# Optimization experiments

Hardware: AMD Instinct MI355X
Metric: run time of the kernel (lower is better)

The kernel has to match this reference:

```python
import jax, jax.numpy as jnp
import numpy as np

N_NODES = 100000

def _graph_conv(x, src, dst, W, b, num_nodes):
    # DGL GraphConv, norm='both', edge_weight=None:
    # h = D_in^{-1/2} * A * (D_out^{-1/2} * x @ W) + b
    ones = jnp.ones(src.shape[0], dtype=x.dtype)
    out_deg = jax.ops.segment_sum(ones, src, num_segments=num_nodes)
    in_deg = jax.ops.segment_sum(ones, dst, num_segments=num_nodes)
    norm_src = jax.lax.rsqrt(jnp.clip(out_deg, 1.0))  # [N]
    norm_dst = jax.lax.rsqrt(jnp.clip(in_deg, 1.0))   # [N]
    h = (x * norm_src[:, None]) @ W                    # [N, out] (weight first: in>=out)
    msg = h[src]                                       # gather over edges [E, out]
    agg = jax.ops.segment_sum(msg, dst, num_segments=num_nodes)  # scatter-add [N, out]
    return agg * norm_dst[:, None] + b


def setup_inputs() -> dict:
    key = jax.random.key(0)
    k = jax.random.split(key, 8)
    N, F, H, C, E = N_NODES, 512, 16, 40, 3200000
    x = jax.random.normal(k[0], (N, F), dtype=jnp.float32)
    edge_src = jax.random.randint(k[1], (E,), 0, N, dtype=jnp.int32)
    edge_dst = jax.random.randint(k[2], (E,), 0, N, dtype=jnp.int32)
    # Glorot-style init for GraphConv weights, zero bias (DGL defaults)
    W1 = jax.random.normal(k[3], (F, H), dtype=jnp.float32) * (1.0 / np.sqrt(F))
    b1 = jnp.zeros((H,), dtype=jnp.float32)
    W2 = jax.random.normal(k[4], (H, C), dtype=jnp.float32) * (1.0 / np.sqrt(H))
    b2 = jnp.zeros((C,), dtype=jnp.float32)
    return {"x": x, "edge_src": edge_src, "edge_dst": edge_dst,
            "W1": W1, "b1": b1, "W2": W2, "b2": b2}


def reference(x, edge_src, edge_dst, W1, b1, W2, b2):
    h = _graph_conv(x, edge_src, edge_dst, W1, b1, N_NODES)
    h = jax.nn.relu(h)
    # dropout p=0.5 is identity in eval mode
    out = _graph_conv(h, edge_src, edge_dst, W2, b2, N_NODES)
    return out
```

## Files before the change

kernel.cpp:

```cpp
#include <hip/hip_runtime.h>

#define F_IN  512
#define H_DIM 16
#define C_OUT 40
#define NBLK_P 256

static inline size_t align_up(size_t x, size_t a) { return (x + a - 1) / a * a; }

__global__ __launch_bounds__(256) void k_pcount(const int* __restrict__ src,
        const int* __restrict__ dst, int E, int chunk, int nbk,
        int* __restrict__ histS, int* __restrict__ histT) {
    __shared__ int hs[512], hd[512];
    for (int i = threadIdx.x; i < 512; i += 256) { hs[i] = 0; hd[i] = 0; }
    __syncthreads();
    int b = blockIdx.x;
    int s = b * chunk, e = min(s + chunk, E);
    for (int i = s + threadIdx.x; i < e; i += 256) {
        atomicAdd(&hs[src[i] >> 8], 1);
        atomicAdd(&hd[dst[i] >> 8], 1);
    }
    __syncthreads();
    for (int i = threadIdx.x; i < nbk; i += 256) {
        histS[i * NBLK_P + b] = hs[i];
        histT[i * NBLK_P + b] = hd[i];
    }
}

__global__ void k_scan1(int* __restrict__ histS, int* __restrict__ histT,
                        int* __restrict__ bsums) {
    __shared__ int tmp[256];
    int* h = blockIdx.y ? histT : histS;
    int* bs = bsums + blockIdx.y * 512;
    int t = threadIdx.x;
    int gid = blockIdx.x * 256 + t;
    int v = h[gid];
    tmp[t] = v;
    __syncthreads();
    for (int off = 1; off < 256; off <<= 1) {
        int add = (t >= off) ? tmp[t - off] : 0;
        __syncthreads();
        tmp[t] += add;
        __syncthreads();
    }
    h[gid] = tmp[t] - v;
    if (t == 255) bs[blockIdx.x] = tmp[255];
}

__global__ void k_scan2(int* __restrict__ bsums, int nb) {
    __shared__ int tmp[512];
    int* bs = bsums + blockIdx.x * 512;
    int t = threadIdx.x;
    int v = (t < nb) ? bs[t] : 0;
    tmp[t] = v;
    __syncthreads();
    for (int off = 1; off < 512; off <<= 1) {
        int add = (t >= off) ? tmp[t - off] : 0;
        __syncthreads();
        tmp[t] += add;
        __syncthreads();
    }
    if (t < nb) bs[t] = tmp[t] - v;
}

__global__ void k_scan3(int* __restrict__ histS, int* __restrict__ histT,
                        const int* __restrict__ bsums) {
    int* h = blockIdx.y ? histT : histS;
    const int* bs = bsums + blockIdx.y * 512;
    h[blockIdx.x * 256 + threadIdx.x] += bs[blockIdx.x];
}

__global__ __launch_bounds__(256) void k_pscat(const int* __restrict__ src,
        const int* __restrict__ dst, int E, int chunk,
        const int* __restrict__ histS, const int* __restrict__ histT,
        unsigned char* __restrict__ srcb, unsigned int* __restrict__ pairsb) {
    __shared__ int cs[512], cd[512];
    for (int i = threadIdx.x; i < 512; i += 256) { cs[i] = 0; cd[i] = 0; }
    __syncthreads();
    int b = blockIdx.x;
    int s = b * chunk, e = min(s + chunk, E);
    for (int i = s + threadIdx.x; i < e; i += 256) {
        int k = src[i];
        int d = dst[i];
        int bks = k >> 8;
        int bkd = d >> 8;
        int rs = atomicAdd(&cs[bks], 1);
        int rd = atomicAdd(&cd[bkd], 1);
        srcb[histS[bks * NBLK_P + b] + rs] = (unsigned char)(k & 255);
        pairsb[histT[bkd * NBLK_P + b] + rd] =
            (unsigned int)k | ((unsigned int)(d & 255) << 24);
    }
}

__global__ __launch_bounds__(256) void k_bbuild(const unsigned char* __restrict__ srcb,
        const unsigned int* __restrict__ pairsb,
        const int* __restrict__ histS, const int* __restrict__ histT,
        int nbk, int E, int N, int* __restrict__ outdeg,
        int* __restrict__ indeg, int* __restrict__ csroff, int* __restrict__ csrsrc) {
    __shared__ int h[256], offs[256], cnt[256], tmp[256];
    int t = threadIdx.x, b = blockIdx.x;
    int node = (b << 8) + t;

    int sstart = histS[b * NBLK_P];
    int send = (b + 1 < nbk) ? histS[(b + 1) * NBLK_P] : E;
    h[t] = 0;
    __syncthreads();
    for (int i = sstart + t; i < send; i += 256)
        atomicAdd(&h[srcb[i]], 1);
    __syncthreads();
    if (node < N) outdeg[node] = h[t];
    __syncthreads();

    int bstart = histT[b * NBLK_P];
    int bend = (b + 1 < nbk) ? histT[(b + 1) * NBLK_P] : E;
    h[t] = 0; cnt[t] = 0;
    __syncthreads();
    for (int i = bstart + t; i < bend; i += 256)
        atomicAdd(&h[pairsb[i] >> 24], 1);
    __syncthreads();
    int v = h[t];
    tmp[t] = v;
    __syncthreads();
    for (int off = 1; off < 256; off <<= 1) {
        int add = (t >= off) ? tmp[t - off] : 0;
        __syncthreads();
        tmp[t] += add;
        __syncthreads();
    }
    offs[t] = tmp[t] - v;
    __syncthreads();
    if (node < N) {
        indeg[node] = v;
        csroff[node] = bstart + offs[t];
    }
    for (int i = bstart + t; i < bend; i += 256) {
        unsigned int p = pairsb[i];
        int l = p >> 24;
        int r = atomicAdd(&cnt[l], 1);
        csrsrc[bstart + offs[l] + r] = (int)(p & 0xFFFFFF);
    }
}

__global__ __launch_bounds__(256) void k_gemm1(const float* __restrict__ x,
        const float* __restrict__ W1, const int* __restrict__ outdeg,
        float* __restrict__ h1, int n) {
    __shared__ float Ws[F_IN * H_DIM];
    for (int i = threadIdx.x; i < F_IN * H_DIM / 4; i += 256)
        ((float4*)Ws)[i] = ((const float4*)W1)[i];
    __syncthreads();

    int row = blockIdx.x * 256 + threadIdx.x;
    if (row >= n) return;
    const float4* xr = (const float4*)(x + (size_t)row * F_IN);
    float ns = rsqrtf(fmaxf((float)outdeg[row], 1.f));

    float acc[H_DIM];
#pragma unroll
    for (int j = 0; j < H_DIM; ++j) acc[j] = 0.f;

    for (int c = 0; c < F_IN / 16; ++c) {
        float4 xv0 = xr[c * 4 + 0];
        float4 xv1 = xr[c * 4 + 1];
        float4 xv2 = xr[c * 4 + 2];
        float4 xv3 = xr[c * 4 + 3];
        float xs[16] = {xv0.x, xv0.y, xv0.z, xv0.w,
                        xv1.x, xv1.y, xv1.z, xv1.w,
                        xv2.x, xv2.y, xv2.z, xv2.w,
                        xv3.x, xv3.y, xv3.z, xv3.w};
#pragma unroll
        for (int kk = 0; kk < 16; ++kk) {
            const float* wr = &Ws[(c * 16 + kk) * H_DIM];
#pragma unroll
            for (int j = 0; j < H_DIM; ++j) acc[j] += xs[kk] * wr[j];
        }
    }

    float4* o = (float4*)(h1 + (size_t)row * H_DIM);
#pragma unroll
    for (int qq = 0; qq < 4; ++qq)
        o[qq] = make_float4(acc[qq * 4 + 0] * ns, acc[qq * 4 + 1] * ns,
                            acc[qq * 4 + 2] * ns, acc[qq * 4 + 3] * ns);
}

__global__ __launch_bounds__(256) void k_agg1(const int* __restrict__ csroff,
        const int* __restrict__ indeg, const int* __restrict__ outdeg,
        const int* __restrict__ csrsrc, const float* __restrict__ h1,
        const float* __restrict__ b1, float* __restrict__ g, int n) {
    int t = threadIdx.x;
    int q = t & 3;
    int lv = t >> 2;
    int v = blockIdx.x * 64 + lv;
    if (v >= n) return;
    int start = csroff[v];
    int len = indeg[v];
    const float4* h4 = (const float4*)h1;
    float4 acc = make_float4(0.f, 0.f, 0.f, 0.f);
    int i = 0;
    for (; i + 4 <= len; i += 4) {
        int s0 = csrsrc[start + i + 0];
        int s1 = csrsrc[start + i + 1];
        int s2 = csrsrc[start + i + 2];
        int s3 = csrsrc[start + i + 3];
        float4 m0 = h4[(size_t)s0 * 4 + q];
        float4 m1 = h4[(size_t)s1 * 4 + q];
        float4 m2 = h4[(size_t)s2 * 4 + q];
        float4 m3 = h4[(size_t)s3 * 4 + q];
        acc.x += m0.x + m1.x + m2.x + m3.x;
        acc.y += m0.y + m1.y + m2.y + m3.y;
        acc.z += m0.z + m1.z + m2.z + m3.z;
        acc.w += m0.w + m1.w + m2.w + m3.w;
    }
    for (; i < len; ++i) {
        int s = csrsrc[start + i];
        float4 m = h4[(size_t)s * 4 + q];
        acc.x += m.x; acc.y += m.y; acc.z += m.z; acc.w += m.w;
    }
    float nd = rsqrtf(fmaxf((float)len, 1.f));
    float ns = rsqrtf(fmaxf((float)outdeg[v], 1.f));
    float4 bb = ((const float4*)b1)[q];
    float4 r;
    r.x = fmaxf(acc.x * nd + bb.x, 0.f) * ns;
    r.y = fmaxf(acc.y * nd + bb.y, 0.f) * ns;
    r.z = fmaxf(acc.z * nd + bb.z, 0.f) * ns;
    r.w = fmaxf(acc.w * nd + bb.w, 0.f) * ns;
    ((float4*)g)[(size_t)v * 4 + q] = r;
}

__global__ __launch_bounds__(256) void k_agg2(const int* __restrict__ csroff,
        const int* __restrict__ indeg, const int* __restrict__ csrsrc,
        const float* __restrict__ gbuf, const float* __restrict__ W2,
        const float* __restrict__ b2, float* __restrict__ out, int n) {
    __shared__ float Ws[H_DIM * C_OUT];
    __shared__ float agg[64][17];
    int t = threadIdx.x;
    for (int i = t; i < H_DIM * C_OUT; i += 256) Ws[i] = W2[i];

    int q = t & 3;
    int lv = t >> 2;
    int v = blockIdx.x * 64 + lv;
    float4 acc = make_float4(0.f, 0.f, 0.f, 0.f);
    if (v < n) {
        int start = csroff[v];
        int len = indeg[v];
        const float4* g4 = (const float4*)gbuf;
        int i = 0;
        for (; i + 4 <= len; i += 4) {
            int s0 = csrsrc[start + i + 0];
            int s1 = csrsrc[start + i + 1];
            int s2 = csrsrc[start + i + 2];
            int s3 = csrsrc[start + i + 3];
            float4 m0 = g4[(size_t)s0 * 4 + q];
            float4 m1 = g4[(size_t)s1 * 4 + q];
            float4 m2 = g4[(size_t)s2 * 4 + q];
            float4 m3 = g4[(size_t)s3 * 4 + q];
            acc.x += m0.x + m1.x + m2.x + m3.x;
            acc.y += m0.y + m1.y + m2.y + m3.y;
            acc.z += m0.z + m1.z + m2.z + m3.z;
            acc.w += m0.w + m1.w + m2.w + m3.w;
        }
        for (; i < len; ++i) {
            int s = csrsrc[start + i];
            float4 m = g4[(size_t)s * 4 + q];
            acc.x += m.x; acc.y += m.y; acc.z += m.z; acc.w += m.w;
        }
    }
    agg[lv][q * 4 + 0] = acc.x;
    agg[lv][q * 4 + 1] = acc.y;
    agg[lv][q * 4 + 2] = acc.z;
    agg[lv][q * 4 + 3] = acc.w;
    __syncthreads();

    for (int idx = t; idx < 64 * C_OUT; idx += 256) {
        int dlv = idx / C_OUT;
        int c = idx % C_OUT;
        int dv = blockIdx.x * 64 + dlv;
        if (dv < n) {
            float s = 0.f;
#pragma unroll
            for (int k = 0; k < H_DIM; ++k) s += agg[dlv][k] * Ws[k * C_OUT + c];
            float nd = rsqrtf(fmaxf((float)indeg[dv], 1.f));
            out[(size_t)dv * C_OUT + c] = s * nd + b2[c];
        }
    }
}

extern "C" void kernel_launch(void* const* d_in, const int* in_sizes, int n_in,
                              void* d_out, int out_size, void* d_ws, size_t ws_size,
                              hipStream_t stream) {
    const float* x  = (const float*)d_in[0];
    const int* esrc = (const int*)d_in[1];
    const int* edst = (const int*)d_in[2];
    const float* W1 = (const float*)d_in[3];
    const float* b1 = (const float*)d_in[4];
    const float* W2 = (const float*)d_in[5];
    const float* b2 = (const float*)d_in[6];
    float* out = (float*)d_out;

    const int N = in_sizes[0] / F_IN;
    const int E = in_sizes[1];
    const int nbk = (N + 255) >> 8;
    const int chunk = (E + NBLK_P - 1) / NBLK_P;

    char* p = (char*)d_ws;
    auto alloc = [&](size_t bytes) -> char* {
        char* r = p; p += align_up(bytes, 256); return r;
    };
    int*  histS  = (int*)alloc((size_t)nbk * NBLK_P * 4);
    int*  histT  = (int*)alloc((size_t)nbk * NBLK_P * 4);
    int*  bsums  = (int*)alloc(1024 * 4);
    unsigned int*  pairsb = (unsigned int*)alloc((size_t)E * 4);
    unsigned char* srcb   = (unsigned char*)alloc((size_t)E);
    int*  csrsrc = (int*)alloc((size_t)E * 4);
    int*  indeg  = (int*)alloc((size_t)N * 4);
    int*  outdeg = (int*)alloc((size_t)N * 4);
    int*  csroff = (int*)alloc((size_t)N * 4);

    float* h1 = (float*)pairsb;
    float* g  = h1 + (size_t)N * H_DIM;

    k_pcount<<<NBLK_P, 256, 0, stream>>>(esrc, edst, E, chunk, nbk, histS, histT);
    k_scan1<<<dim3(nbk, 2), 256, 0, stream>>>(histS, histT, bsums);
    k_scan2<<<2, 512, 0, stream>>>(bsums, nbk);
    k_scan3<<<dim3(nbk, 2), 256, 0, stream>>>(histS, histT, bsums);
    k_pscat<<<NBLK_P, 256, 0, stream>>>(esrc, edst, E, chunk, histS, histT,
                                        srcb, pairsb);
    k_bbuild<<<nbk, 256, 0, stream>>>(srcb, pairsb, histS, histT, nbk, E, N,
                                      outdeg, indeg, csroff, csrsrc);

    k_gemm1<<<(N + 255) / 256, 256, 0, stream>>>(x, W1, outdeg, h1, N);
    int nb64 = (N + 63) / 64;
    k_agg1<<<nb64, 256, 0, stream>>>(csroff, indeg, outdeg, csrsrc, h1, b1, g, N);
    k_agg2<<<nb64, 256, 0, stream>>>(csroff, indeg, csrsrc, g, W2, b2, out, N);
}
```

Measured before the change: 279.6 us.

## Fuse edge histogram with first GEMM and fold scan3 into consumers

The dense x@W1 GEMM now runs as extra blocks inside the edge histogram kernel, so the compute-heavy GEMM overlaps with the atomic-bound counting pass and no longer waits for degrees. The out-degree normalisation moves into k_bbuild, which rescales h1 in place. The scan3 pass is removed: consumers add the block sums on the fly. The partition count doubles to 512, and h1 gets its own buffer instead of aliasing pairsb. The cost is an extra read-modify-write of h1 and extra index arithmetic in the scatter.

```diff
diff --git a/kernel.cpp b/kernel.cpp
--- a/kernel.cpp
+++ b/kernel.cpp
@@ -3,34 +3,78 @@
 #define F_IN  512
 #define H_DIM 16
 #define C_OUT 40
-#define NBLK_P 256
+#define NBLK_P 512
 
 static inline size_t align_up(size_t x, size_t a) { return (x + a - 1) / a * a; }
 
-__global__ __launch_bounds__(256) void k_pcount(const int* __restrict__ src,
+__global__ __launch_bounds__(256) void k_fused1(const int* __restrict__ src,
         const int* __restrict__ dst, int E, int chunk, int nbk,
-        int* __restrict__ histS, int* __restrict__ histT) {
-    __shared__ int hs[512], hd[512];
-    for (int i = threadIdx.x; i < 512; i += 256) { hs[i] = 0; hd[i] = 0; }
-    __syncthreads();
-    int b = blockIdx.x;
-    int s = b * chunk, e = min(s + chunk, E);
-    for (int i = s + threadIdx.x; i < e; i += 256) {
-        atomicAdd(&hs[src[i] >> 8], 1);
-        atomicAdd(&hd[dst[i] >> 8], 1);
-    }
-    __syncthreads();
-    for (int i = threadIdx.x; i < nbk; i += 256) {
-        histS[i * NBLK_P + b] = hs[i];
-        histT[i * NBLK_P + b] = hd[i];
-    }
+        int* __restrict__ histS, int* __restrict__ histT,
+        const float* __restrict__ x, const float* __restrict__ W1,
+        float* __restrict__ h1, int n) {
+    __shared__ float smem[F_IN * H_DIM];
+    int t = threadIdx.x;
+
+    if (blockIdx.x < NBLK_P) {
+        int* hs = (int*)smem;
+        int* hd = hs + 512;
+        for (int i = t; i < 1024; i += 256) hs[i] = 0;
+        __syncthreads();
+        int b = blockIdx.x;
+        int s = b * chunk, e = min(s + chunk, E);
+        for (int i = s + t; i < e; i += 256) {
+            atomicAdd(&hs[src[i] >> 8], 1);
+            atomicAdd(&hd[dst[i] >> 8], 1);
+        }
+        __syncthreads();
+        for (int i = t; i < nbk; i += 256) {
+            histS[i * NBLK_P + b] = hs[i];
+            histT[i * NBLK_P + b] = hd[i];
+        }
+        return;
+    }
+
+    for (int i = t; i < F_IN * H_DIM / 4; i += 256)
+        ((float4*)smem)[i] = ((const float4*)W1)[i];
+    __syncthreads();
+
+    int row = (blockIdx.x - NBLK_P) * 256 + t;
+    if (row >= n) return;
+    const float4* xr = (const float4*)(x + (size_t)row * F_IN);
+
+    float acc[H_DIM];
+#pragma unroll
+    for (int j = 0; j < H_DIM; ++j) acc[j] = 0.f;
+
+    for (int c = 0; c < F_IN / 16; ++c) {
+        float4 xv0 = xr[c * 4 + 0];
+        float4 xv1 = xr[c * 4 + 1];
+        float4 xv2 = xr[c * 4 + 2];
+        float4 xv3 = xr[c * 4 + 3];
+        float xs[16] = {xv0.x, xv0.y, xv0.z, xv0.w,
+                        xv1.x, xv1.y, xv1.z, xv1.w,
+                        xv2.x, xv2.y, xv2.z, xv2.w,
+                        xv3.x, xv3.y, xv3.z, xv3.w};
+#pragma unroll
+        for (int kk = 0; kk < 16; ++kk) {
+            const float* wr = &smem[(c * 16 + kk) * H_DIM];
+#pragma unroll
+            for (int j = 0; j < H_DIM; ++j) acc[j] += xs[kk] * wr[j];
+        }
+    }
+
+    float4* o = (float4*)(h1 + (size_t)row * H_DIM);
+#pragma unroll
+    for (int qq = 0; qq < 4; ++qq)
+        o[qq] = make_float4(acc[qq * 4 + 0], acc[qq * 4 + 1],
+                            acc[qq * 4 + 2], acc[qq * 4 + 3]);
 }
 
 __global__ void k_scan1(int* __restrict__ histS, int* __restrict__ histT,
                         int* __restrict__ bsums) {
     __shared__ int tmp[256];
     int* h = blockIdx.y ? histT : histS;
-    int* bs = bsums + blockIdx.y * 512;
+    int* bs = bsums + blockIdx.y * 1024;
     int t = threadIdx.x;
     int gid = blockIdx.x * 256 + t;
     int v = h[gid];
@@ -47,33 +91,29 @@
 }
 
 __global__ void k_scan2(int* __restrict__ bsums, int nb) {
-    __shared__ int tmp[512];
-    int* bs = bsums + blockIdx.x * 512;
+    __shared__ int tmp[1024];
+    int* bs = bsums + blockIdx.x * 1024;
     int t = threadIdx.x;
     int v = (t < nb) ? bs[t] : 0;
     tmp[t] = v;
     __syncthreads();
-    for (int off = 1; off < 512; off <<= 1) {
+    for (int off = 1; off < 1024; off <<= 1) {
         int add = (t >= off) ? tmp[t - off] : 0;
         __syncthreads();
         tmp[t] += add;
         __syncthreads();
     }
     if (t < nb) bs[t] = tmp[t] - v;
-}
-
-__global__ void k_scan3(int* __restrict__ histS, int* __restrict__ histT,
-                        const int* __restrict__ bsums) {
-    int* h = blockIdx.y ? histT : histS;
-    const int* bs = bsums + blockIdx.y * 512;
-    h[blockIdx.x * 256 + threadIdx.x] += bs[blockIdx.x];
 }
 
 __global__ __launch_bounds__(256) void k_pscat(const int* __restrict__ src,
         const int* __restrict__ dst, int E, int chunk,
         const int* __restrict__ histS, const int* __restrict__ histT,
+        const int* __restrict__ bsums,
         unsigned char* __restrict__ srcb, unsigned int* __restrict__ pairsb) {
     __shared__ int cs[512], cd[512];
+    const int* bsS = bsums;
+    const int* bsT = bsums + 1024;
     for (int i = threadIdx.x; i < 512; i += 256) { cs[i] = 0; cd[i] = 0; }
     __syncthreads();
     int b = blockIdx.x;
@@ -85,8 +125,10 @@
         int bkd = d >> 8;
         int rs = atomicAdd(&cs[bks], 1);
         int rd = atomicAdd(&cd[bkd], 1);
-        srcb[histS[bks * NBLK_P + b] + rs] = (unsigned char)(k & 255);
-        pairsb[histT[bkd * NBLK_P + b] + rd] =
+        int is = bks * NBLK_P + b;
+        int id = bkd * NBLK_P + b;
+        srcb[histS[is] + bsS[is >> 8] + rs] = (unsigned char)(k & 255);
+        pairsb[histT[id] + bsT[id >> 8] + rd] =
             (unsigned int)k | ((unsigned int)(d & 255) << 24);
     }
 }
@@ -94,24 +136,38 @@
 __global__ __launch_bounds__(256) void k_bbuild(const unsigned char* __restrict__ srcb,
         const unsigned int* __restrict__ pairsb,
         const int* __restrict__ histS, const int* __restrict__ histT,
-        int nbk, int E, int N, int* __restrict__ outdeg,
-        int* __restrict__ indeg, int* __restrict__ csroff, int* __restrict__ csrsrc) {
+        const int* __restrict__ bsums, int nbk, int E, int N,
+        int* __restrict__ outdeg, int* __restrict__ indeg,
+        int* __restrict__ csroff, int* __restrict__ csrsrc,
+        float* __restrict__ h1) {
     __shared__ int h[256], offs[256], cnt[256], tmp[256];
+    const int* bsS = bsums;
+    const int* bsT = bsums + 1024;
     int t = threadIdx.x, b = blockIdx.x;
     int node = (b << 8) + t;
 
-    int sstart = histS[b * NBLK_P];
-    int send = (b + 1 < nbk) ? histS[(b + 1) * NBLK_P] : E;
+    int sstart = histS[b * NBLK_P] + bsS[(b * NBLK_P) >> 8];
+    int send = (b + 1 < nbk) ? histS[(b + 1) * NBLK_P] + bsS[((b + 1) * NBLK_P) >> 8] : E;
     h[t] = 0;
     __syncthreads();
     for (int i = sstart + t; i < send; i += 256)
         atomicAdd(&h[srcb[i]], 1);
     __syncthreads();
-    if (node < N) outdeg[node] = h[t];
-    __syncthreads();
-
-    int bstart = histT[b * NBLK_P];
-    int bend = (b + 1 < nbk) ? histT[(b + 1) * NBLK_P] : E;
+    int odeg = h[t];
+    __syncthreads();
+    if (node < N) {
+        outdeg[node] = odeg;
+        float ns = rsqrtf(fmaxf((float)odeg, 1.f));
+        float4* r = (float4*)(h1 + (size_t)node * H_DIM);
+#pragma unroll
+        for (int qq = 0; qq < 4; ++qq) {
+            float4 v = r[qq];
+            r[qq] = make_float4(v.x * ns, v.y * ns, v.z * ns, v.w * ns);
+        }
+    }
+
+    int bstart = histT[b * NBLK_P] + bsT[(b * NBLK_P) >> 8];
+    int bend = (b + 1 < nbk) ? histT[(b + 1) * NBLK_P] + bsT[((b + 1) * NBLK_P) >> 8] : E;
     h[t] = 0; cnt[t] = 0;
     __syncthreads();
     for (int i = bstart + t; i < bend; i += 256)
@@ -138,47 +194,6 @@
         int r = atomicAdd(&cnt[l], 1);
         csrsrc[bstart + offs[l] + r] = (int)(p & 0xFFFFFF);
     }
-}
-
-__global__ __launch_bounds__(256) void k_gemm1(const float* __restrict__ x,
-        const float* __restrict__ W1, const int* __restrict__ outdeg,
-        float* __restrict__ h1, int n) {
-    __shared__ float Ws[F_IN * H_DIM];
-    for (int i = threadIdx.x; i < F_IN * H_DIM / 4; i += 256)
-        ((float4*)Ws)[i] = ((const float4*)W1)[i];
-    __syncthreads();
-
-    int row = blockIdx.x * 256 + threadIdx.x;
-    if (row >= n) return;
-    const float4* xr = (const float4*)(x + (size_t)row * F_IN);
-    float ns = rsqrtf(fmaxf((float)outdeg[row], 1.f));
-
-    float acc[H_DIM];
-#pragma unroll
-    for (int j = 0; j < H_DIM; ++j) acc[j] = 0.f;
-
-    for (int c = 0; c < F_IN / 16; ++c) {
-        float4 xv0 = xr[c * 4 + 0];
-        float4 xv1 = xr[c * 4 + 1];
-        float4 xv2 = xr[c * 4 + 2];
-        float4 xv3 = xr[c * 4 + 3];
-        float xs[16] = {xv0.x, xv0.y, xv0.z, xv0.w,
-                        xv1.x, xv1.y, xv1.z, xv1.w,
-                        xv2.x, xv2.y, xv2.z, xv2.w,
-                        xv3.x, xv3.y, xv3.z, xv3.w};
-#pragma unroll
-        for (int kk = 0; kk < 16; ++kk) {
-            const float* wr = &Ws[(c * 16 + kk) * H_DIM];
-#pragma unroll
-            for (int j = 0; j < H_DIM; ++j) acc[j] += xs[kk] * wr[j];
-        }
-    }
-
-    float4* o = (float4*)(h1 + (size_t)row * H_DIM);
-#pragma unroll
-    for (int qq = 0; qq < 4; ++qq)
-        o[qq] = make_float4(acc[qq * 4 + 0] * ns, acc[qq * 4 + 1] * ns,
-                            acc[qq * 4 + 2] * ns, acc[qq * 4 + 3] * ns);
 }
 
 __global__ __launch_bounds__(256) void k_agg1(const int* __restrict__ csroff,
@@ -299,6 +314,7 @@
     const int E = in_sizes[1];
     const int nbk = (N + 255) >> 8;
     const int chunk = (E + NBLK_P - 1) / NBLK_P;
+    const int nscan = nbk * NBLK_P / 256;
 
     char* p = (char*)d_ws;
     auto alloc = [&](size_t bytes) -> char* {
@@ -306,27 +322,27 @@
     };
     int*  histS  = (int*)alloc((size_t)nbk * NBLK_P * 4);
     int*  histT  = (int*)alloc((size_t)nbk * NBLK_P * 4);
-    int*  bsums  = (int*)alloc(1024 * 4);
+    int*  bsums  = (int*)alloc(2048 * 4);
     unsigned int*  pairsb = (unsigned int*)alloc((size_t)E * 4);
     unsigned char* srcb   = (unsigned char*)alloc((size_t)E);
     int*  csrsrc = (int*)alloc((size_t)E * 4);
+    float* h1    = (float*)alloc((size_t)N * H_DIM * 4);
     int*  indeg  = (int*)alloc((size_t)N * 4);
     int*  outdeg = (int*)alloc((size_t)N * 4);
     int*  csroff = (int*)alloc((size_t)N * 4);
 
-    float* h1 = (float*)pairsb;
-    float* g  = h1 + (size_t)N * H_DIM;
-
-    k_pcount<<<NBLK_P, 256, 0, stream>>>(esrc, edst, E, chunk, nbk, histS, histT);
-    k_scan1<<<dim3(nbk, 2), 256, 0, stream>>>(histS, histT, bsums);
-    k_scan2<<<2, 512, 0, stream>>>(bsums, nbk);
-    k_scan3<<<dim3(nbk, 2), 256, 0, stream>>>(histS, histT, bsums);
+    float* g = (float*)pairsb;
+
+    int ngemm = (N + 255) / 256;
+    k_fused1<<<NBLK_P + ngemm, 256, 0, stream>>>(esrc, edst, E, chunk, nbk,
+                                                 histS, histT, x, W1, h1, N);
+    k_scan1<<<dim3(nscan, 2), 256, 0, stream>>>(histS, histT, bsums);
+    k_scan2<<<2, 1024, 0, stream>>>(bsums, nscan);
     k_pscat<<<NBLK_P, 256, 0, stream>>>(esrc, edst, E, chunk, histS, histT,
-                                        srcb, pairsb);
-    k_bbuild<<<nbk, 256, 0, stream>>>(srcb, pairsb, histS, histT, nbk, E, N,
-                                      outdeg, indeg, csroff, csrsrc);
-
-    k_gemm1<<<(N + 255) / 256, 256, 0, stream>>>(x, W1, outdeg, h1, N);
+                                        bsums, srcb, pairsb);
+    k_bbuild<<<nbk, 256, 0, stream>>>(srcb, pairsb, histS, histT, bsums,
+                                      nbk, E, N, outdeg, indeg, csroff, csrsrc, h1);
+
     int nb64 = (N + 63) / 64;
     k_agg1<<<nb64, 256, 0, stream>>>(csroff, indeg, outdeg, csrsrc, h1, b1, g, N);
     k_agg2<<<nb64, 256, 0, stream>>>(csroff, indeg, csrsrc, g, W2, b2, out, N);
```

Measured after the change: 289.3 us. +3.5%, slower.
